# Kernel optimization log

Hardware: AMD Instinct MI355X
Metric: run time of the kernel (lower is better)

The kernel has to match this reference:

```python
import jax, jax.numpy as jnp
import numpy as np


def _layernorm(x, gamma, beta, eps=1e-5):
    mu = jnp.mean(x, axis=-1, keepdims=True)
    var = jnp.mean(jnp.square(x - mu), axis=-1, keepdims=True)
    return (x - mu) * jax.lax.rsqrt(var + eps) * gamma + beta


def _sparse_ternary_linear(x, W, b, sparsity):
    # Ternary quantization (BitNet-style): per-tensor scale = mean(|W|),
    # dynamic sparsity: zero out the `sparsity` fraction of smallest-|W| entries,
    # remaining weights -> sign(W), rescaled by `scale`.
    absW = jnp.abs(W)
    scale = jnp.mean(absW)
    thresh = jnp.quantile(absW, sparsity)
    q = jnp.sign(W) * (absW > thresh).astype(W.dtype)  # ternary {-1,0,+1}
    return jnp.einsum('bnd,hd->bnh', x, q * scale) + b


def setup_inputs() -> dict:
    key = jax.random.key(0)
    ks = jax.random.split(key, 8)
    B, N, D, H = 32, 1024, 768, 3072
    return {
        'x': jax.random.normal(ks[0], (B, N, D), dtype=jnp.float32),
        'ln1_g': jnp.ones((D,), jnp.float32),
        'ln1_b': jnp.zeros((D,), jnp.float32),
        'W1': jax.random.normal(ks[1], (H, D), dtype=jnp.float32) * 0.02,
        'b1': jnp.zeros((H,), jnp.float32),
        'ln2_g': jnp.ones((H,), jnp.float32),
        'ln2_b': jnp.zeros((H,), jnp.float32),
        'W2': jax.random.normal(ks[2], (D, H), dtype=jnp.float32) * 0.02,
        'b2': jnp.zeros((D,), jnp.float32),
        'sparsity': jnp.float32(0.5),
    }


def reference(x, ln1_g, ln1_b, W1, b1, ln2_g, ln2_b, W2, b2, sparsity):
    h = _layernorm(x, ln1_g, ln1_b)
    h = _sparse_ternary_linear(h, W1, b1, sparsity)
    h = jax.nn.gelu(h)  # dropout=0.0 (eval): identity
    h = _layernorm(h, ln2_g, ln2_b)
    h = _sparse_ternary_linear(h, W2, b2, sparsity)
    return h
```

## Files before the change

kernel.cpp:

```cpp
#include <hip/hip_runtime.h>
#include <math.h>

using f32x4    = __attribute__((ext_vector_type(4))) float;
using short8   = __attribute__((ext_vector_type(8))) short;
using ushort8  = __attribute__((ext_vector_type(8))) unsigned short;
using ushort4v = __attribute__((ext_vector_type(4))) unsigned short;
using u32x4    = __attribute__((ext_vector_type(4))) unsigned int;

#define D_DIM 768
#define H_DIM 3072

#define L1_BITS 14
#define L1_SIZE 16384

static const size_t HIST1_OFF = 0;
static const size_t HIST2_OFF = 131072;
static const size_t HIST3_OFF = 139264;
static const size_t SUM_OFF   = 147456;
static const size_t THR_OFF   = 147472;
static const size_t META_OFF  = 147488;
static const size_t MU2A_OFF  = 147616;
static const size_t SS2A_OFF  = 278688;
static const size_t ZERO_BYTES= 409760;
static const size_t S1_OFF    = 409760;
static const size_t S2_OFF    = 412832;
static const size_t MU2_OFF   = 415904;
static const size_t RS2_OFF   = 546976;
static const size_t WQ1_OFF   = 5242880;
static const size_t WQ2_OFF   = 9961472;
static const size_t H1_OFF    = 16777216;

__device__ __forceinline__ unsigned short f2bf(float f) {
    unsigned u = __float_as_uint(f);
    u += 0x7fffu + ((u >> 16) & 1u);
    return (unsigned short)(u >> 16);
}
__device__ __forceinline__ float bf2f(unsigned short s) {
    return __uint_as_float(((unsigned)s) << 16);
}

__device__ __forceinline__ void gload16(const unsigned short* g, unsigned short* l) {
    __builtin_amdgcn_global_load_lds(
        (const __attribute__((address_space(1))) unsigned int*)g,
        (__attribute__((address_space(3))) unsigned int*)l, 16, 0, 0);
}

__global__ void hist_abs_kernel(const float* __restrict__ W1, int n1,
                                const float* __restrict__ W2, int n2,
                                unsigned* __restrict__ hist, double* __restrict__ sums) {
    __shared__ unsigned lh[L1_SIZE];
    const int t = blockIdx.y;
    const float* W = t ? W2 : W1;
    const int n = t ? n2 : n1;
    unsigned* hg = hist + (size_t)t * L1_SIZE;

    for (int i = threadIdx.x; i < L1_SIZE; i += 256) lh[i] = 0;
    __syncthreads();

    int tid = blockIdx.x * blockDim.x + threadIdx.x;
    int stride = gridDim.x * blockDim.x;
    double local = 0.0;
    int n4 = n >> 2;
    for (int i = tid; i < n4; i += stride) {
        f32x4 w = ((const f32x4*)W)[i];
#pragma unroll
        for (int j = 0; j < 4; j++) {
            float a = fabsf(w[j]);
            local += (double)a;
            atomicAdd(&lh[__float_as_uint(a) >> (32 - L1_BITS)], 1u);
        }
    }
    for (int i = (n4 << 2) + tid; i < n; i += stride) {
        float a = fabsf(W[i]);
        local += (double)a;
        atomicAdd(&lh[__float_as_uint(a) >> (32 - L1_BITS)], 1u);
    }
    __syncthreads();
    for (int i = threadIdx.x; i < L1_SIZE; i += 256) {
        unsigned c = lh[i];
        if (c) atomicAdd(&hg[i], c);
    }
#pragma unroll
    for (int off = 32; off >= 1; off >>= 1) local += __shfl_down(local, off);
    if ((threadIdx.x & 63) == 0) atomicAdd(&sums[t], local);
}

__global__ void scan1_kernel(const unsigned* __restrict__ hist, unsigned* __restrict__ meta_u,
                             const float* __restrict__ sparsity, int n1, int n2) {
    __shared__ unsigned partial[256];
    __shared__ unsigned basearr[256];
    for (int t = 0; t < 2; t++) {
        const unsigned* h = hist + (size_t)t * L1_SIZE;
        int n = t ? n2 : n1;
        double p = (double)(*sparsity) * (double)(n - 1);
        unsigned kA = (unsigned)floor(p);
        unsigned kB = kA + 1; if (kB > (unsigned)(n - 1)) kB = (unsigned)(n - 1);
        int b0 = threadIdx.x * 64;
        unsigned s_local = 0;
#pragma unroll
        for (int b = 0; b < 64; b += 4) {
            u32x4 v = *(const u32x4*)&h[b0 + b];
            s_local += v[0] + v[1] + v[2] + v[3];
        }
        partial[threadIdx.x] = s_local;
        __syncthreads();
        if (threadIdx.x == 0) {
            unsigned run = 0;
            for (int i = 0; i < 256; i++) { unsigned tmp = partial[i]; basearr[i] = run; run += tmp; }
        }
        __syncthreads();
        unsigned cumbase = basearr[threadIdx.x];
        for (int s = 0; s < 2; s++) {
            unsigned rank = s ? kB : kA;
            if (rank >= cumbase && rank < cumbase + s_local) {
                unsigned cum = cumbase;
                for (int b = 0; b < 64; b++) {
                    unsigned c = h[b0 + b];
                    if (rank < cum + c) { meta_u[s * 4 + t] = (unsigned)(b0 + b); meta_u[s * 4 + 2 + t] = rank - cum; break; }
                    cum += c;
                }
            }
        }
        __syncthreads();
    }
}

template<int LVL>
__global__ void histN_kernel(const float* __restrict__ W1, int n1,
                             const float* __restrict__ W2, int n2,
                             const unsigned* __restrict__ meta_u, unsigned* __restrict__ histo) {
    __shared__ unsigned hA[512], hB[512];
    const int t = blockIdx.y;
    const float* W = t ? W2 : W1;
    const int n = t ? n2 : n1;
    for (int i = threadIdx.x; i < 512; i += 256) { hA[i] = 0; hB[i] = 0; }
    __syncthreads();
    const int inbase = (LVL == 2) ? 0 : 16;
    unsigned pa = meta_u[inbase + 0 + t], pb = meta_u[inbase + 4 + t];
    int tid = blockIdx.x * blockDim.x + threadIdx.x;
    int stride = gridDim.x * blockDim.x;
    int n4 = n >> 2;
    for (int i = tid; i < n4; i += stride) {
        f32x4 w = ((const f32x4*)W)[i];
#pragma unroll
        for (int j = 0; j < 4; j++) {
            unsigned u = __float_as_uint(fabsf(w[j]));
            unsigned pf  = (LVL == 2) ? (u >> 18) : (u >> 9);
            unsigned idx = (LVL == 2) ? ((u >> 9) & 0x1FFu) : (u & 0x1FFu);
            if (pf == pa) atomicAdd(&hA[idx], 1u);
            if (pf == pb) atomicAdd(&hB[idx], 1u);
        }
    }
    for (int i = (n4 << 2) + tid; i < n; i += stride) {
        unsigned u = __float_as_uint(fabsf(W[i]));
        unsigned pf  = (LVL == 2) ? (u >> 18) : (u >> 9);
        unsigned idx = (LVL == 2) ? ((u >> 9) & 0x1FFu) : (u & 0x1FFu);
        if (pf == pa) atomicAdd(&hA[idx], 1u);
        if (pf == pb) atomicAdd(&hB[idx], 1u);
    }
    __syncthreads();
    for (int i = threadIdx.x; i < 512; i += 256) {
        unsigned a = hA[i]; if (a) atomicAdd(&histo[(size_t)(t * 2 + 0) * 512 + i], a);
        unsigned b = hB[i]; if (b) atomicAdd(&histo[(size_t)(t * 2 + 1) * 512 + i], b);
    }
}

__global__ void scan_mid_kernel(const unsigned* __restrict__ histo, unsigned* __restrict__ meta_u) {
    int wave = threadIdx.x >> 6, lane = threadIdx.x & 63;
    int s = wave >> 1, t = wave & 1;
    const unsigned* h = histo + (size_t)(t * 2 + s) * 512;
    unsigned rank = meta_u[s * 4 + 2 + t];
    unsigned pfx  = meta_u[s * 4 + t];
    u32x4 ca = *(const u32x4*)&h[lane * 8];
    u32x4 cb = *(const u32x4*)&h[lane * 8 + 4];
    unsigned cc[8] = {ca[0], ca[1], ca[2], ca[3], cb[0], cb[1], cb[2], cb[3]};
    unsigned csum = cc[0] + cc[1] + cc[2] + cc[3] + cc[4] + cc[5] + cc[6] + cc[7];
    unsigned inc = csum;
#pragma unroll
    for (int off = 1; off < 64; off <<= 1) {
        unsigned v = __shfl_up(inc, off, 64);
        if (lane >= off) inc += v;
    }
    unsigned pre = inc - csum;
    if (rank >= pre && rank < pre + csum) {
        unsigned cum = pre, rem = 0, bucket = 0; bool found = false;
#pragma unroll
        for (int j = 0; j < 8; j++) {
            if (!found) {
                if (rank < cum + cc[j]) { bucket = lane * 8 + j; rem = rank - cum; found = true; }
                else cum += cc[j];
            }
        }
        meta_u[16 + s * 4 + t] = (pfx << 9) | bucket;
        meta_u[16 + s * 4 + 2 + t] = rem;
    }
}

__global__ void scan_fin_kernel(const unsigned* __restrict__ histo, unsigned* __restrict__ meta_u,
                                const double* __restrict__ sums, const float* __restrict__ sparsity,
                                double* __restrict__ thr, int n1, int n2) {
    __shared__ unsigned vbs[4];
    int wave = threadIdx.x >> 6, lane = threadIdx.x & 63;
    int s = wave >> 1, t = wave & 1;
    const unsigned* h = histo + (size_t)(t * 2 + s) * 512;
    unsigned rank = meta_u[16 + s * 4 + 2 + t];
    unsigned pfx  = meta_u[16 + s * 4 + t];
    u32x4 ca = *(const u32x4*)&h[lane * 8];
    u32x4 cb = *(const u32x4*)&h[lane * 8 + 4];
    unsigned cc[8] = {ca[0], ca[1], ca[2], ca[3], cb[0], cb[1], cb[2], cb[3]};
    unsigned csum = cc[0] + cc[1] + cc[2] + cc[3] + cc[4] + cc[5] + cc[6] + cc[7];
    unsigned inc = csum;
#pragma unroll
    for (int off = 1; off < 64; off <<= 1) {
        unsigned v = __shfl_up(inc, off, 64);
        if (lane >= off) inc += v;
    }
    unsigned pre = inc - csum;
    if (rank >= pre && rank < pre + csum) {
        unsigned cum = pre, bucket = 0; bool found = false;
#pragma unroll
        for (int j = 0; j < 8; j++) {
            if (!found) {
                if (rank < cum + cc[j]) { bucket = lane * 8 + j; found = true; }
                else cum += cc[j];
            }
        }
        vbs[t * 2 + s] = (pfx << 9) | bucket;
    }
    __syncthreads();
    if (threadIdx.x < 2) {
        int tt = threadIdx.x;
        int n = tt ? n2 : n1;
        double a = (double)__uint_as_float(vbs[tt * 2 + 0]);
        double b = (double)__uint_as_float(vbs[tt * 2 + 1]);
        double p = (double)(*sparsity) * (double)(n - 1);
        double tfr = p - floor(p);
        double th = (tfr >= 0.5) ? (b - (b - a) * (1.0 - tfr)) : (a + (b - a) * tfr);
        thr[tt] = th;
        ((float*)meta_u)[24 + tt] = (float)(sums[tt] / (double)n);
    }
}

__global__ void quantize_kernel(const float* __restrict__ W1, int n1,
                                const float* __restrict__ W2, int n2,
                                const double* __restrict__ thr, const float* __restrict__ g2,
                                unsigned short* __restrict__ wq1, unsigned short* __restrict__ wq2) {
    int tid = blockIdx.x * blockDim.x + threadIdx.x;
    int stride = gridDim.x * blockDim.x;
    for (int t = 0; t < 2; t++) {
        const float* W = t ? W2 : W1;
        unsigned short* O = t ? wq2 : wq1;
        int n = t ? n2 : n1;
        double th = thr[t];
        int n4 = n >> 2;
        for (int i = tid; i < n4; i += stride) {
            f32x4 w = ((const f32x4*)W)[i];
            ushort4v q;
            if (t == 0) {
#pragma unroll
                for (int j = 0; j < 4; j++) {
                    unsigned short v = 0;
                    if ((double)fabsf(w[j]) > th) v = (w[j] > 0.f) ? 0x3F80u : 0xBF80u;
                    q[j] = v;
                }
            } else {
                int k4 = (i % (H_DIM / 4)) * 4;
                f32x4 g = *(const f32x4*)&g2[k4];
#pragma unroll
                for (int j = 0; j < 4; j++) {
                    unsigned short v = 0;
                    if ((double)fabsf(w[j]) > th) {
                        unsigned short gb = f2bf(g[j]);
                        v = (w[j] > 0.f) ? gb : (unsigned short)(gb ^ 0x8000u);
                    }
                    q[j] = v;
                }
            }
            ((ushort4v*)O)[i] = q;
        }
    }
}

__global__ void colsum_kernel(const float* __restrict__ W2, const double* __restrict__ thr,
                              const float* __restrict__ g2, const float* __restrict__ bln2,
                              float* __restrict__ S1, float* __restrict__ S2) {
    int wave = threadIdx.x >> 6, lane = threadIdx.x & 63;
    int c = blockIdx.x * 4 + wave;
    const float* wr = W2 + (size_t)c * H_DIM;
    double th = thr[1];
    float s1 = 0.f, s2 = 0.f;
    for (int k = lane * 4; k < H_DIM; k += 256) {
        f32x4 w = *(const f32x4*)&wr[k];
        f32x4 g = *(const f32x4*)&g2[k];
        f32x4 b = *(const f32x4*)&bln2[k];
#pragma unroll
        for (int j = 0; j < 4; j++) {
            if ((double)fabsf(w[j]) > th) {
                float sg = (w[j] > 0.f) ? 1.f : -1.f;
                s1 += sg * bf2f(f2bf(g[j]));
                s2 += sg * b[j];
            }
        }
    }
#pragma unroll
    for (int off = 32; off >= 1; off >>= 1) { s1 += __shfl_xor(s1, off); s2 += __shfl_xor(s2, off); }
    if (lane == 0) { S1[c] = s1; S2[c] = s2; }
}

__global__ void ln1_apply_kernel(const float* __restrict__ x, const float* __restrict__ g,
                                 const float* __restrict__ b, unsigned short* __restrict__ xn, int M) {
    int wave = threadIdx.x >> 6, lane = threadIdx.x & 63;
    int row = blockIdx.x * 4 + wave;
    if (row >= M) return;
    const float* xr = x + (size_t)row * D_DIM;
    f32x4 xv[3];
    float s = 0.f, s2 = 0.f;
#pragma unroll
    for (int i = 0; i < 3; i++) {
        xv[i] = *(const f32x4*)&xr[lane * 4 + i * 256];
#pragma unroll
        for (int j = 0; j < 4; j++) { s += xv[i][j]; s2 += xv[i][j] * xv[i][j]; }
    }
#pragma unroll
    for (int off = 32; off >= 1; off >>= 1) { s += __shfl_xor(s, off); s2 += __shfl_xor(s2, off); }
    float m = s / (float)D_DIM;
    float var = s2 / (float)D_DIM - m * m;
    float rs = 1.f / sqrtf(var + 1e-5f);
    unsigned short* xo = xn + (size_t)row * D_DIM;
#pragma unroll
    for (int i = 0; i < 3; i++) {
        int k = lane * 4 + i * 256;
        f32x4 gg = *(const f32x4*)&g[k];
        f32x4 bb = *(const f32x4*)&b[k];
        ushort4v o;
#pragma unroll
        for (int j = 0; j < 4; j++) o[j] = f2bf((xv[i][j] - m) * rs * gg[j] + bb[j]);
        *(ushort4v*)&xo[k] = o;
    }
}

__global__ void ln2stats_kernel(const float* __restrict__ sa, const float* __restrict__ sb,
                                float* __restrict__ mu, float* __restrict__ rs, int M) {
    int i = blockIdx.x * 256 + threadIdx.x;
    if (i >= M) return;
    float m = sa[i] / (float)H_DIM;
    float var = sb[i] / (float)H_DIM - m * m;
    mu[i] = m;
    rs[i] = 1.f / sqrtf(var + 1e-5f);
}

template<int KD, int NBN, int EPI>
__launch_bounds__(256)
__global__ void gemm_tern_kernel(const unsigned short* __restrict__ A,
                                 const unsigned short* __restrict__ Bq,
                                 const float* __restrict__ bias,
                                 const float* __restrict__ meta_f, int sidx,
                                 void* __restrict__ outp,
                                 float* __restrict__ rsum_g, float* __restrict__ rsum2_g,
                                 const float* __restrict__ mu2, const float* __restrict__ rs2,
                                 const float* __restrict__ S1, const float* __restrict__ S2) {
    __shared__ unsigned short As[128 * 64];
    __shared__ unsigned short Bs[128 * 64];
    const int bid = blockIdx.x;
    const int xcd = bid & 7, idx = bid >> 3;
    const int mb = (idx / NBN) * 8 + xcd;
    const int nb = idx % NBN;
    const int m0 = mb * 128, n0 = nb * 128;
    const float scale = meta_f[sidx];
    const int tt = threadIdx.x, lane = tt & 63, wave = tt >> 6;
    const int wm = (wave & 1) * 64, wn = (wave >> 1) * 64;
    const int l16 = lane & 15, l4 = lane >> 4;
    const int srow = tt >> 3, schunk = tt & 7;

    f32x4 acc[4][4];
#pragma unroll
    for (int mi = 0; mi < 4; mi++)
#pragma unroll
        for (int ni = 0; ni < 4; ni++) acc[mi][ni] = (f32x4){0.f, 0.f, 0.f, 0.f};

    for (int k0 = 0; k0 < KD; k0 += 64) {
#pragma unroll
        for (int r = 0; r < 4; r++) {
            int row = r * 32 + srow;
            int sc = (schunk ^ (row & 7)) << 3;
            gload16(&A[(size_t)(m0 + row) * KD + k0 + sc], &As[(size_t)tt * 8 + r * 2048]);
        }
#pragma unroll
        for (int r = 0; r < 4; r++) {
            int row = r * 32 + srow;
            int sc = (schunk ^ (row & 7)) << 3;
            gload16(&Bq[(size_t)(n0 + row) * KD + k0 + sc], &Bs[(size_t)tt * 8 + r * 2048]);
        }
        __syncthreads();
#pragma unroll
        for (int ks = 0; ks < 2; ks++) {
            short8 af[4], bf_[4];
#pragma unroll
            for (int i = 0; i < 4; i++) {
                int ar = wm + i * 16 + l16;
                af[i] = *(const short8*)&As[ar * 64 + (((ks * 4 + l4) ^ (ar & 7)) << 3)];
                int br = wn + i * 16 + l16;
                bf_[i] = *(const short8*)&Bs[br * 64 + (((ks * 4 + l4) ^ (br & 7)) << 3)];
            }
#pragma unroll
            for (int mi = 0; mi < 4; mi++)
#pragma unroll
                for (int ni = 0; ni < 4; ni++)
                    acc[mi][ni] = __builtin_amdgcn_mfma_f32_16x16x32_bf16(af[mi], bf_[ni], acc[mi][ni], 0, 0, 0);
        }
        __syncthreads();
    }

    if constexpr (EPI == 1) {
        float rs_[4][4], rq_[4][4];
#pragma unroll
        for (int mi = 0; mi < 4; mi++)
#pragma unroll
            for (int j = 0; j < 4; j++) { rs_[mi][j] = 0.f; rq_[mi][j] = 0.f; }
#pragma unroll
        for (int ni = 0; ni < 4; ni++) {
            int col = n0 + wn + ni * 16 + l16;
            float bl = bias[col];
#pragma unroll
            for (int mi = 0; mi < 4; mi++)
#pragma unroll
                for (int j = 0; j < 4; j++) {
                    int row = m0 + wm + mi * 16 + l4 * 4 + j;
                    float v = acc[mi][ni][j] * scale + bl;
                    float y = 1.5957691216f * (v + 0.044715f * v * v * v);
                    float e = exp2f(-1.4426950409f * y);
                    float gel = v / (1.f + e);
                    unsigned short hb = f2bf(gel);
                    float gv = bf2f(hb);
                    ((unsigned short*)outp)[(size_t)row * H_DIM + col] = hb;
                    rs_[mi][j] += gv;
                    rq_[mi][j] += gv * gv;
                }
        }
#pragma unroll
        for (int mi = 0; mi < 4; mi++)
#pragma unroll
            for (int j = 0; j < 4; j++) {
                float s = rs_[mi][j], q = rq_[mi][j];
#pragma unroll
                for (int off = 1; off <= 8; off <<= 1) { s += __shfl_xor(s, off); q += __shfl_xor(q, off); }
                if (l16 == 0) {
                    int row = m0 + wm + mi * 16 + l4 * 4 + j;
                    atomicAdd(&rsum_g[row], s);
                    atomicAdd(&rsum2_g[row], q);
                }
            }
    } else {
#pragma unroll
        for (int mi = 0; mi < 4; mi++)
#pragma unroll
            for (int j = 0; j < 4; j++) {
                int row = m0 + wm + mi * 16 + l4 * 4 + j;
                float mr = mu2[row], rr = rs2[row];
#pragma unroll
                for (int ni = 0; ni < 4; ni++) {
                    int col = n0 + wn + ni * 16 + l16;
                    float v = scale * (rr * (acc[mi][ni][j] - mr * S1[col]) + S2[col]) + bias[col];
                    ((float*)outp)[(size_t)row * D_DIM + col] = v;
                }
            }
    }
}

extern "C" void kernel_launch(void* const* d_in, const int* in_sizes, int n_in,
                              void* d_out, int out_size, void* d_ws, size_t ws_size,
                              hipStream_t stream) {
    const float* x    = (const float*)d_in[0];
    const float* ln1g = (const float*)d_in[1];
    const float* ln1b = (const float*)d_in[2];
    const float* W1   = (const float*)d_in[3];
    const float* b1   = (const float*)d_in[4];
    const float* ln2g = (const float*)d_in[5];
    const float* ln2b = (const float*)d_in[6];
    const float* W2   = (const float*)d_in[7];
    const float* b2   = (const float*)d_in[8];
    const float* sp   = (const float*)d_in[9];
    const int n1 = in_sizes[3], n2 = in_sizes[7];
    const int M = in_sizes[0] / D_DIM;

    char* ws = (char*)d_ws;
    unsigned* hist1 = (unsigned*)(ws + HIST1_OFF);
    unsigned* hist2 = (unsigned*)(ws + HIST2_OFF);
    unsigned* hist3 = (unsigned*)(ws + HIST3_OFF);
    double*   sums  = (double*)(ws + SUM_OFF);
    double*   thr   = (double*)(ws + THR_OFF);
    unsigned* meta_u = (unsigned*)(ws + META_OFF);
    float*    meta_f = (float*)(ws + META_OFF);
    float* mu2a = (float*)(ws + MU2A_OFF);
    float* ss2a = (float*)(ws + SS2A_OFF);
    float* S1   = (float*)(ws + S1_OFF);
    float* S2   = (float*)(ws + S2_OFF);
    float* mu2  = (float*)(ws + MU2_OFF);
    float* rs2  = (float*)(ws + RS2_OFF);
    unsigned short* wq1 = (unsigned short*)(ws + WQ1_OFF);
    unsigned short* wq2 = (unsigned short*)(ws + WQ2_OFF);
    unsigned short* h1  = (unsigned short*)(ws + H1_OFF);
    unsigned short* xn  = (unsigned short*)d_out;

    hipMemsetAsync(d_ws, 0, ZERO_BYTES, stream);
    hist_abs_kernel<<<dim3(512, 2), 256, 0, stream>>>(W1, n1, W2, n2, hist1, sums);
    scan1_kernel<<<1, 256, 0, stream>>>(hist1, meta_u, sp, n1, n2);
    histN_kernel<2><<<dim3(256, 2), 256, 0, stream>>>(W1, n1, W2, n2, meta_u, hist2);
    scan_mid_kernel<<<1, 256, 0, stream>>>(hist2, meta_u);
    histN_kernel<3><<<dim3(256, 2), 256, 0, stream>>>(W1, n1, W2, n2, meta_u, hist3);
    scan_fin_kernel<<<1, 256, 0, stream>>>(hist3, meta_u, sums, sp, thr, n1, n2);
    quantize_kernel<<<2048, 256, 0, stream>>>(W1, n1, W2, n2, thr, ln2g, wq1, wq2);
    colsum_kernel<<<D_DIM / 4, 256, 0, stream>>>(W2, thr, ln2g, ln2b, S1, S2);
    ln1_apply_kernel<<<M / 4, 256, 0, stream>>>(x, ln1g, ln1b, xn, M);
    gemm_tern_kernel<D_DIM, 24, 1><<<24 * (M / 128), 256, 0, stream>>>(
        xn, wq1, b1, meta_f, 24, h1, mu2a, ss2a, nullptr, nullptr, nullptr, nullptr);
    ln2stats_kernel<<<M / 256, 256, 0, stream>>>(mu2a, ss2a, mu2, rs2, M);
    gemm_tern_kernel<H_DIM, 6, 2><<<6 * (M / 128), 256, 0, stream>>>(
        h1, wq2, b2, meta_f, 25, d_out, nullptr, nullptr, mu2, rs2, S1, S2);
}
```

Baseline: 987.8 us.

## Replace atomic row-stat accumulation with per-slot partial buffers and plain 2D grid

```diff
diff --git a/kernel.cpp b/kernel.cpp
--- a/kernel.cpp
+++ b/kernel.cpp
@@ -19,16 +19,16 @@
 static const size_t SUM_OFF   = 147456;
 static const size_t THR_OFF   = 147472;
 static const size_t META_OFF  = 147488;
-static const size_t MU2A_OFF  = 147616;
-static const size_t SS2A_OFF  = 278688;
-static const size_t ZERO_BYTES= 409760;
-static const size_t S1_OFF    = 409760;
-static const size_t S2_OFF    = 412832;
-static const size_t MU2_OFF   = 415904;
-static const size_t RS2_OFF   = 546976;
+static const size_t ZERO_BYTES= 147616;
+static const size_t S1_OFF    = 147616;
+static const size_t S2_OFF    = 150688;
+static const size_t MU2_OFF   = 153760;
+static const size_t RS2_OFF   = 284832;
 static const size_t WQ1_OFF   = 5242880;
 static const size_t WQ2_OFF   = 9961472;
 static const size_t H1_OFF    = 16777216;
+static const size_t PARTS_DOUT_OFF = 50331648;
+static const size_t PARTQ_DOUT_OFF = 50331648 + 6291456;
 
 __device__ __forceinline__ unsigned short f2bf(float f) {
     unsigned u = __float_as_uint(f);
@@ -339,33 +339,39 @@
     }
 }
 
-__global__ void ln2stats_kernel(const float* __restrict__ sa, const float* __restrict__ sb,
+__global__ void ln2stats_kernel(const float* __restrict__ parts, const float* __restrict__ partq,
                                 float* __restrict__ mu, float* __restrict__ rs, int M) {
     int i = blockIdx.x * 256 + threadIdx.x;
     if (i >= M) return;
-    float m = sa[i] / (float)H_DIM;
-    float var = sb[i] / (float)H_DIM - m * m;
+    const float* ps = parts + (size_t)i * 48;
+    const float* pq = partq + (size_t)i * 48;
+    float s = 0.f, q = 0.f;
+#pragma unroll
+    for (int j = 0; j < 48; j += 4) {
+        f32x4 a = *(const f32x4*)&ps[j];
+        f32x4 b = *(const f32x4*)&pq[j];
+        s += a[0] + a[1] + a[2] + a[3];
+        q += b[0] + b[1] + b[2] + b[3];
+    }
+    float m = s / (float)H_DIM;
+    float var = q / (float)H_DIM - m * m;
     mu[i] = m;
     rs[i] = 1.f / sqrtf(var + 1e-5f);
 }
 
-template<int KD, int NBN, int EPI>
+template<int KD, int EPI>
 __launch_bounds__(256)
 __global__ void gemm_tern_kernel(const unsigned short* __restrict__ A,
                                  const unsigned short* __restrict__ Bq,
                                  const float* __restrict__ bias,
                                  const float* __restrict__ meta_f, int sidx,
                                  void* __restrict__ outp,
-                                 float* __restrict__ rsum_g, float* __restrict__ rsum2_g,
+                                 float* __restrict__ parts, float* __restrict__ partq,
                                  const float* __restrict__ mu2, const float* __restrict__ rs2,
                                  const float* __restrict__ S1, const float* __restrict__ S2) {
     __shared__ unsigned short As[128 * 64];
     __shared__ unsigned short Bs[128 * 64];
-    const int bid = blockIdx.x;
-    const int xcd = bid & 7, idx = bid >> 3;
-    const int mb = (idx / NBN) * 8 + xcd;
-    const int nb = idx % NBN;
-    const int m0 = mb * 128, n0 = nb * 128;
+    const int m0 = blockIdx.y * 128, n0 = blockIdx.x * 128;
     const float scale = meta_f[sidx];
     const int tt = threadIdx.x, lane = tt & 63, wave = tt >> 6;
     const int wm = (wave & 1) * 64, wn = (wave >> 1) * 64;
@@ -437,6 +443,7 @@
                     rq_[mi][j] += gv * gv;
                 }
         }
+        const int slot = blockIdx.x * 2 + (wave >> 1);
 #pragma unroll
         for (int mi = 0; mi < 4; mi++)
 #pragma unroll
@@ -446,8 +453,8 @@
                 for (int off = 1; off <= 8; off <<= 1) { s += __shfl_xor(s, off); q += __shfl_xor(q, off); }
                 if (l16 == 0) {
                     int row = m0 + wm + mi * 16 + l4 * 4 + j;
-                    atomicAdd(&rsum_g[row], s);
-                    atomicAdd(&rsum2_g[row], q);
+                    parts[(size_t)row * 48 + slot] = s;
+                    partq[(size_t)row * 48 + slot] = q;
                 }
             }
     } else {
@@ -491,8 +498,6 @@
     double*   thr   = (double*)(ws + THR_OFF);
     unsigned* meta_u = (unsigned*)(ws + META_OFF);
     float*    meta_f = (float*)(ws + META_OFF);
-    float* mu2a = (float*)(ws + MU2A_OFF);
-    float* ss2a = (float*)(ws + SS2A_OFF);
     float* S1   = (float*)(ws + S1_OFF);
     float* S2   = (float*)(ws + S2_OFF);
     float* mu2  = (float*)(ws + MU2_OFF);
@@ -501,6 +506,8 @@
     unsigned short* wq2 = (unsigned short*)(ws + WQ2_OFF);
     unsigned short* h1  = (unsigned short*)(ws + H1_OFF);
     unsigned short* xn  = (unsigned short*)d_out;
+    float* parts = (float*)((char*)d_out + PARTS_DOUT_OFF);
+    float* partq = (float*)((char*)d_out + PARTQ_DOUT_OFF);
 
     hipMemsetAsync(d_ws, 0, ZERO_BYTES, stream);
     hist_abs_kernel<<<dim3(512, 2), 256, 0, stream>>>(W1, n1, W2, n2, hist1, sums);
@@ -512,9 +519,9 @@
     quantize_kernel<<<2048, 256, 0, stream>>>(W1, n1, W2, n2, thr, ln2g, wq1, wq2);
     colsum_kernel<<<D_DIM / 4, 256, 0, stream>>>(W2, thr, ln2g, ln2b, S1, S2);
     ln1_apply_kernel<<<M / 4, 256, 0, stream>>>(x, ln1g, ln1b, xn, M);
-    gemm_tern_kernel<D_DIM, 24, 1><<<24 * (M / 128), 256, 0, stream>>>(
-        xn, wq1, b1, meta_f, 24, h1, mu2a, ss2a, nullptr, nullptr, nullptr, nullptr);
-    ln2stats_kernel<<<M / 256, 256, 0, stream>>>(mu2a, ss2a, mu2, rs2, M);
-    gemm_tern_kernel<H_DIM, 6, 2><<<6 * (M / 128), 256, 0, stream>>>(
+    gemm_tern_kernel<D_DIM, 1><<<dim3(H_DIM / 128, M / 128), 256, 0, stream>>>(
+        xn, wq1, b1, meta_f, 24, h1, parts, partq, nullptr, nullptr, nullptr, nullptr);
+    ln2stats_kernel<<<M / 256, 256, 0, stream>>>(parts, partq, mu2, rs2, M);
+    gemm_tern_kernel<H_DIM, 2><<<dim3(D_DIM / 128, M / 128), 256, 0, stream>>>(
         h1, wq2, b2, meta_f, 25, d_out, nullptr, nullptr, mu2, rs2, S1, S2);
 }
```

New measurement: 811.1 us. -17.9%, faster.
